# Optimization experiments

Measured on AMD Instinct MI355X. Metric: run time of the kernel, lower is better.

Reference implementation:

```python
import jax, jax.numpy as jnp
import numpy as np

S, I, IN_DIM, PROJ_DIM, OUT_DIM = 128, 384, 256, 32, 128
LN_EPS = 1e-5


def _layer_norm(x):
    # utils.normalize in OmegaFold: F.layer_norm over last dim, no affine params
    mu = jnp.mean(x, axis=-1, keepdims=True)
    var = jnp.var(x, axis=-1, keepdims=True)
    return (x - mu) * jax.lax.rsqrt(var + LN_EPS)


def setup_inputs() -> dict:
    key = jax.random.key(0)
    k0, k1, k2, k3 = jax.random.split(key, 4)
    node_repr = jax.random.normal(k0, (S, I, IN_DIM), dtype=jnp.float32)
    mask = (jax.random.uniform(k1, (S, I)) < 0.9).astype(jnp.float32)
    W_proj = jax.random.normal(k2, (IN_DIM, 2 * PROJ_DIM), dtype=jnp.float32) / np.sqrt(IN_DIM)
    b_proj = jnp.zeros((2 * PROJ_DIM,), dtype=jnp.float32)
    out_weights = jax.random.normal(k3, (PROJ_DIM, PROJ_DIM, OUT_DIM), dtype=jnp.float32) * 0.02
    out_bias = jnp.zeros((OUT_DIM,), dtype=jnp.float32)
    return {
        "node_repr": node_repr,
        "mask": mask,
        "W_proj": W_proj,
        "b_proj": b_proj,
        "out_weights": out_weights,
        "out_bias": out_bias,
    }


def reference(node_repr, mask, W_proj, b_proj, out_weights, out_bias):
    # LayerNorm (no affine) -> linear projection to 2*proj_dim
    x = _layer_norm(node_repr)                       # [s, i, in_dim]
    act = x @ W_proj + b_proj                        # [s, i, 2d]
    m = mask[..., None]                              # [s, i, 1]
    act = act * m
    # mask-pair counts: einsum('si,sj->ij')
    norm = jnp.einsum("si,sj->ij", mask, mask)[..., None]  # [i, j, 1]
    l = act[..., :PROJ_DIM]                          # [s, i, d]
    r = act[..., PROJ_DIM:]                          # [s, j, e]
    # outer-product mean over s, then contract (d,e)->f with the 3-tensor
    outer = jnp.einsum("sid,sje->ijde", l, r)        # [i, j, d, e]
    out = jnp.einsum("ijde,def->ijf", outer, out_weights) + out_bias  # [i, j, f]
    return out / (norm + 0.001)
```

## Files before the change

kernel.cpp:

```cpp
#include <hip/hip_runtime.h>

#define S_DIM 128
#define I_DIM 384
#define IN_DIM 256
#define PD 32
#define ODIM 128

typedef __attribute__((ext_vector_type(8))) __bf16 bf16x8;
typedef __attribute__((ext_vector_type(4))) float f32x4;

#define MFMA16(a, b, c) __builtin_amdgcn_mfma_f32_16x16x32_bf16((a), (b), (c), 0, 0, 0)

__device__ inline unsigned short f2bf(float f) {
    unsigned int u = __builtin_bit_cast(unsigned int, f);
    unsigned int r = (u + 0x7FFFu + ((u >> 16) & 1u)) >> 16;
    return (unsigned short)r;
}

__global__ void prep_cast(const float* __restrict__ Wp, const float* __restrict__ W2,
                          unsigned short* __restrict__ WpT, unsigned short* __restrict__ W2t) {
    int t = blockIdx.x * 256 + threadIdx.x;
    if (t < 64 * 256) {
        int f = t >> 8, k = t & 255;
        WpT[t] = f2bf(Wp[k * 64 + f]);
    }
    if (t < 128 * 1024) {
        int f = t >> 10, de = t & 1023;
        int e = de >> 5, d = de & 31;
        W2t[t] = f2bf(W2[(d * 32 + e) * 128 + f]);
    }
}

__global__ void norm_kernel(const float* __restrict__ mask, float* __restrict__ invn) {
    __shared__ float mi[S_DIM][16];
    __shared__ float mj[S_DIM][16];
    int t = threadIdx.x;
    int i0 = blockIdx.y * 16, j0 = blockIdx.x * 16;
    for (int p = 0; p < 8; ++p) {
        int s = p * 16 + (t >> 4);
        int c = t & 15;
        mi[s][c] = mask[s * I_DIM + i0 + c];
        mj[s][c] = mask[s * I_DIM + j0 + c];
    }
    __syncthreads();
    int ii = t >> 4, jj = t & 15;
    float acc = 0.f;
#pragma unroll 8
    for (int s = 0; s < S_DIM; ++s) acc += mi[s][ii] * mj[s][jj];
    invn[(i0 + ii) * I_DIM + (j0 + jj)] = 1.0f / (acc + 0.001f);
}

__global__ __launch_bounds__(256, 2) void ln_proj(const float* __restrict__ x,
                                                  const float* __restrict__ mask,
                                                  const float* __restrict__ bias,
                                                  const unsigned short* __restrict__ WpT_g,
                                                  unsigned short* __restrict__ lT,
                                                  unsigned short* __restrict__ rT) {
    __shared__ unsigned short xsh[64 * 264];
    __shared__ unsigned short wpT[64 * 264];
    int t = threadIdx.x;
    int w = t >> 6, lane = t & 63;
    int i = blockIdx.x >> 1;
    int s0 = (blockIdx.x & 1) * 64;

    {
        int f = t >> 2, kq = (t & 3) * 64;
#pragma unroll
        for (int p = 0; p < 8; ++p) {
            int k = kq + p * 8;
            *(uint4*)&wpT[f * 264 + k] = *(const uint4*)&WpT_g[f * 256 + k];
        }
    }

    float4 vbuf[4];
#pragma unroll
    for (int p = 0; p < 4; ++p)
        vbuf[p] = *(const float4*)(x + ((size_t)(s0 + w * 16 + p) * I_DIM + i) * IN_DIM + lane * 4);

    for (int it = 0; it < 16; ++it) {
        float4 v = vbuf[it & 3];
        if (it + 4 < 16)
            vbuf[it & 3] = *(const float4*)(x + ((size_t)(s0 + w * 16 + it + 4) * I_DIM + i) * IN_DIM + lane * 4);
        float s1 = v.x + v.y + v.z + v.w;
        float s2 = v.x * v.x + v.y * v.y + v.z * v.z + v.w * v.w;
#pragma unroll
        for (int off = 32; off >= 1; off >>= 1) {
            s1 += __shfl_xor(s1, off);
            s2 += __shfl_xor(s2, off);
        }
        float mu = s1 * (1.f / 256.f);
        float var = s2 * (1.f / 256.f) - mu * mu;
        float rs = rsqrtf(var + 1e-5f);
        unsigned int h0 = f2bf((v.x - mu) * rs);
        unsigned int h1 = f2bf((v.y - mu) * rs);
        unsigned int h2 = f2bf((v.z - mu) * rs);
        unsigned int h3 = f2bf((v.w - mu) * rs);
        uint2 pk;
        pk.x = h0 | (h1 << 16);
        pk.y = h2 | (h3 << 16);
        *(uint2*)&xsh[(w * 16 + it) * 264 + lane * 4] = pk;
    }
    __syncthreads();

    int l15 = lane & 15, q = lane >> 4;
    f32x4 acc[4];
#pragma unroll
    for (int nt = 0; nt < 4; ++nt) acc[nt] = (f32x4){0.f, 0.f, 0.f, 0.f};

    for (int k0 = 0; k0 < 256; k0 += 32) {
        bf16x8 a = *(bf16x8*)&xsh[(w * 16 + l15) * 264 + k0 + q * 8];
#pragma unroll
        for (int nt = 0; nt < 4; ++nt) {
            bf16x8 b = *(bf16x8*)&wpT[(nt * 16 + l15) * 264 + k0 + q * 8];
            acc[nt] = MFMA16(a, b, acc[nt]);
        }
    }

    float mval[4];
#pragma unroll
    for (int reg = 0; reg < 4; ++reg)
        mval[reg] = mask[(size_t)(s0 + w * 16 + q * 4 + reg) * I_DIM + i];

    __syncthreads();
    unsigned short* trsh = xsh;

#pragma unroll
    for (int nt = 0; nt < 4; ++nt) {
        int f = nt * 16 + l15;
        float bv = bias[f];
        unsigned int lo = (unsigned int)f2bf((acc[nt][0] + bv) * mval[0]) |
                          ((unsigned int)f2bf((acc[nt][1] + bv) * mval[1]) << 16);
        unsigned int hi = (unsigned int)f2bf((acc[nt][2] + bv) * mval[2]) |
                          ((unsigned int)f2bf((acc[nt][3] + bv) * mval[3]) << 16);
        uint2 pk; pk.x = lo; pk.y = hi;
        *(uint2*)&trsh[f * 72 + w * 16 + q * 4] = pk;
    }
    __syncthreads();

    {
        int fr = t >> 2, so = (t & 3) * 16;
        unsigned short* dst = ((fr < 32) ? lT : rT) + ((size_t)(i * 32 + (fr & 31)) * 128 + s0 + so);
        *(uint4*)dst = *(uint4*)&trsh[fr * 72 + so];
        *(uint4*)(dst + 8) = *(uint4*)&trsh[fr * 72 + so + 8];
    }
}

__global__ __launch_bounds__(256, 4) void outer_kernel(const unsigned short* __restrict__ lT,
                                                       const unsigned short* __restrict__ rT,
                                                       unsigned short* __restrict__ Gp,
                                                       int ib0) {
    __shared__ unsigned short sh[128 * 136];
    int t = threadIdx.x;
    int bx = blockIdx.x, by = blockIdx.y;
    int colL0 = (ib0 + by) * 128, colR0 = bx * 128;
    int w = t >> 6, lane = t & 63, l15 = lane & 15, q = lane >> 4;

    const unsigned short* lbase = lT + (size_t)(colL0 + w * 32 + l15) * 128 + q * 8;
    bf16x8 a0 = *(const bf16x8*)(lbase);
    bf16x8 a1 = *(const bf16x8*)(lbase + 16 * 128);

    {
        int m0 = t >> 3, c0 = (t & 7) * 8;
        const unsigned short* rbase = rT + (size_t)(colR0 + m0) * 128 + c0;
#pragma unroll
        for (int p = 0; p < 4; ++p) {
            *(uint4*)&sh[(m0 + p * 32) * 136 + c0] = *(const uint4*)(rbase + (size_t)p * 32 * 128);
            *(uint4*)&sh[(m0 + p * 32) * 136 + c0 + 64] = *(const uint4*)(rbase + (size_t)p * 32 * 128 + 64);
        }
    }
    __syncthreads();

    f32x4 acc[2][8];
#pragma unroll
    for (int mt = 0; mt < 2; ++mt)
#pragma unroll
        for (int nt = 0; nt < 8; ++nt) acc[mt][nt] = (f32x4){0.f, 0.f, 0.f, 0.f};

#pragma unroll
    for (int k0 = 0; k0 < 4; ++k0) {
        bf16x8 na0 = a0, na1 = a1;
        if (k0 < 3) {
            na0 = *(const bf16x8*)(lbase + (k0 + 1) * 32);
            na1 = *(const bf16x8*)(lbase + 16 * 128 + (k0 + 1) * 32);
        }
#pragma unroll
        for (int nt = 0; nt < 8; ++nt) {
            bf16x8 b = *(bf16x8*)&sh[(nt * 16 + l15) * 136 + k0 * 32 + q * 8];
            acc[0][nt] = MFMA16(a0, b, acc[0][nt]);
            acc[1][nt] = MFMA16(a1, b, acc[1][nt]);
        }
        a0 = na0; a1 = na1;
    }
    __syncthreads();

#pragma unroll
    for (int mt = 0; mt < 2; ++mt) {
        int rowb = w * 32 + mt * 16 + q * 4;
        int chnk = rowb >> 3;
        int win = rowb & 7;
#pragma unroll
        for (int nt = 0; nt < 8; ++nt) {
            int col = nt * 16 + l15;
            int cs = chnk ^ (col >> 5);
            unsigned int lo = (unsigned int)f2bf(acc[mt][nt][0]) | ((unsigned int)f2bf(acc[mt][nt][1]) << 16);
            unsigned int hi = (unsigned int)f2bf(acc[mt][nt][2]) | ((unsigned int)f2bf(acc[mt][nt][3]) << 16);
            uint2 pk; pk.x = lo; pk.y = hi;
            *(uint2*)&sh[col * 136 + cs * 8 + win] = pk;
        }
    }
    __syncthreads();

#pragma unroll
    for (int p8 = 0; p8 < 8; ++p8) {
        int g = p8 * 256 + t;
        int pair_loc = g >> 7;
        int c16 = g & 127;
        int i_loc = pair_loc >> 2, j_loc = pair_loc & 3;
        int e = c16 >> 2;
        int n = j_loc * 32 + e;
        int cs = (i_loc * 4 + (c16 & 3)) ^ j_loc;
        uint4 v = *(uint4*)&sh[n * 136 + cs * 8];
        size_t row = (size_t)(by * 4 + i_loc) * I_DIM + bx * 4 + j_loc;
        *(uint4*)&Gp[row * 1024 + (size_t)c16 * 8] = v;
    }
}

__global__ __launch_bounds__(256, 4) void contract_kernel(const unsigned short* __restrict__ Gp,
                                                          const unsigned short* __restrict__ W2t,
                                                          const float* __restrict__ invn,
                                                          const float* __restrict__ out_bias,
                                                          float* __restrict__ out,
                                                          int pair0) {
    __shared__ unsigned short Ash[2][64 * 40];
    int t = threadIdx.x;
    int w = t >> 6, lane = t & 63, l15 = lane & 15, q = lane >> 4;
    int p0 = blockIdx.x * 64;

    int sr = t >> 2, sc = (t & 3) * 8;
    const unsigned short* agp = Gp + (size_t)(p0 + sr) * 1024 + sc;
    *(uint4*)&Ash[0][sr * 40 + sc] = *(const uint4*)(agp);

    f32x4 acc[4][2];
#pragma unroll
    for (int mt = 0; mt < 4; ++mt) {
        acc[mt][0] = (f32x4){0.f, 0.f, 0.f, 0.f};
        acc[mt][1] = (f32x4){0.f, 0.f, 0.f, 0.f};
    }
    const unsigned short* wb0 = W2t + (size_t)(w * 32 + l15) * 1024 + q * 8;
    const unsigned short* wb1 = wb0 + 16 * 1024;

    bf16x8 b0c = *(const bf16x8*)(wb0);
    bf16x8 b1c = *(const bf16x8*)(wb1);
    __syncthreads();

    for (int k0 = 0; k0 < 32; ++k0) {
        int cur = k0 & 1;
        uint4 nxtA;
        bf16x8 b0n = b0c, b1n = b1c;
        if (k0 < 31) {
            nxtA = *(const uint4*)(agp + (k0 + 1) * 32);
            b0n = *(const bf16x8*)(wb0 + (k0 + 1) * 32);
            b1n = *(const bf16x8*)(wb1 + (k0 + 1) * 32);
        }
        bf16x8 a[4];
#pragma unroll
        for (int mt = 0; mt < 4; ++mt)
            a[mt] = *(bf16x8*)&Ash[cur][(mt * 16 + l15) * 40 + q * 8];
#pragma unroll
        for (int mt = 0; mt < 4; ++mt) {
            acc[mt][0] = MFMA16(a[mt], b0c, acc[mt][0]);
            acc[mt][1] = MFMA16(a[mt], b1c, acc[mt][1]);
        }
        if (k0 < 31) *(uint4*)&Ash[1 - cur][sr * 40 + sc] = nxtA;
        b0c = b0n; b1c = b1n;
        __syncthreads();
    }

#pragma unroll
    for (int u = 0; u < 2; ++u) {
        int f = w * 32 + u * 16 + l15;
        float bv = out_bias[f];
#pragma unroll
        for (int mt = 0; mt < 4; ++mt) {
#pragma unroll
            for (int reg = 0; reg < 4; ++reg) {
                int pl = pair0 + p0 + mt * 16 + q * 4 + reg;
                out[(size_t)pl * 128 + f] = (acc[mt][u][reg] + bv) * invn[pl];
            }
        }
    }
}

extern "C" void kernel_launch(void* const* d_in, const int* in_sizes, int n_in,
                              void* d_out, int out_size, void* d_ws, size_t ws_size,
                              hipStream_t stream) {
    const float* node = (const float*)d_in[0];
    const float* mask = (const float*)d_in[1];
    const float* Wp   = (const float*)d_in[2];
    const float* bp   = (const float*)d_in[3];
    const float* W2   = (const float*)d_in[4];
    const float* bo   = (const float*)d_in[5];
    float* out = (float*)d_out;

    char* ws = (char*)d_ws;
    unsigned short* lT  = (unsigned short*)(ws);
    unsigned short* rT  = (unsigned short*)(ws + 3145728);
    unsigned short* W2t = (unsigned short*)(ws + 6291456);
    unsigned short* WpT = (unsigned short*)(ws + 6553600);
    float*          inv = (float*)(ws + 6586368);
    unsigned short* Gp  = (unsigned short*)(ws + 8388608);

    int slab_i = 96;
    while (slab_i > 12 && 8388608ull + (size_t)slab_i * 384 * 1024 * 2 > ws_size) slab_i >>= 1;
    int nslab = 384 / slab_i;

    hipLaunchKernelGGL(prep_cast, dim3(512), dim3(256), 0, stream, Wp, W2, WpT, W2t);
    hipLaunchKernelGGL(norm_kernel, dim3(24, 24), dim3(256), 0, stream, mask, inv);
    hipLaunchKernelGGL(ln_proj, dim3(768), dim3(256), 0, stream, node, mask, bp, WpT, lT, rT);

    for (int s = 0; s < nslab; ++s) {
        hipLaunchKernelGGL(outer_kernel, dim3(96, slab_i / 4), dim3(256), 0, stream,
                           lT, rT, Gp, s * (slab_i / 4));
        hipLaunchKernelGGL(contract_kernel, dim3(slab_i * 384 / 64), dim3(256), 0, stream,
                           Gp, W2t, inv, bo, out, s * slab_i * I_DIM);
    }
}
```

Measured before the change: 332.3 us.

## Fuse outer-product and weight contraction into one kernel keeping pairs in LDS

Merges the outer-product kernel and the contraction kernel into a single kernel. Each block computes a 8x4 tile of (i,j) pairs, stores the 1024-wide outer products as bf16 in swizzled shared memory, then contracts against W2 with the K dimension split across the four waves. Partial sums are reduced through LDS before the bias and normalisation are applied. This removes the large Gp intermediate written to and read back from global memory, plus the slab launch loop. In exchange it uses 64KB of LDS and more registers, lowering occupancy to two blocks, and each block reloads W2 from global or cache.

```diff
diff --git a/kernel.cpp b/kernel.cpp
--- a/kernel.cpp
+++ b/kernel.cpp
@@ -145,23 +145,23 @@
     }
 }
 
-__global__ __launch_bounds__(256, 4) void outer_kernel(const unsigned short* __restrict__ lT,
+__global__ __launch_bounds__(256, 2) void fused_kernel(const unsigned short* __restrict__ lT,
                                                        const unsigned short* __restrict__ rT,
-                                                       unsigned short* __restrict__ Gp,
-                                                       int ib0) {
-    __shared__ unsigned short sh[128 * 136];
+                                                       const unsigned short* __restrict__ W2t,
+                                                       const float* __restrict__ invn,
+                                                       const float* __restrict__ out_bias,
+                                                       float* __restrict__ out) {
+    __shared__ unsigned short sh[32768];
     int t = threadIdx.x;
-    int bx = blockIdx.x, by = blockIdx.y;
-    int colL0 = (ib0 + by) * 128, colR0 = bx * 128;
     int w = t >> 6, lane = t & 63, l15 = lane & 15, q = lane >> 4;
-
-    const unsigned short* lbase = lT + (size_t)(colL0 + w * 32 + l15) * 128 + q * 8;
-    bf16x8 a0 = *(const bf16x8*)(lbase);
-    bf16x8 a1 = *(const bf16x8*)(lbase + 16 * 128);
+    int bx = blockIdx.x;
+    int by = blockIdx.y;
+    int wm = w >> 1, wn = w & 1;
+    char* shb = (char*)sh;
 
     {
         int m0 = t >> 3, c0 = (t & 7) * 8;
-        const unsigned short* rbase = rT + (size_t)(colR0 + m0) * 128 + c0;
+        const unsigned short* rbase = rT + (size_t)(bx * 128 + m0) * 128 + c0;
 #pragma unroll
         for (int p = 0; p < 4; ++p) {
             *(uint4*)&sh[(m0 + p * 32) * 136 + c0] = *(const uint4*)(rbase + (size_t)p * 32 * 128);
@@ -170,124 +170,107 @@
     }
     __syncthreads();
 
-    f32x4 acc[2][8];
-#pragma unroll
-    for (int mt = 0; mt < 2; ++mt)
-#pragma unroll
-        for (int nt = 0; nt < 8; ++nt) acc[mt][nt] = (f32x4){0.f, 0.f, 0.f, 0.f};
+    f32x4 acc[8][4];
+#pragma unroll
+    for (int mt = 0; mt < 8; ++mt)
+#pragma unroll
+        for (int nt = 0; nt < 4; ++nt) acc[mt][nt] = (f32x4){0.f, 0.f, 0.f, 0.f};
+
+    const unsigned short* lbase = lT + (size_t)(by * 256 + wm * 128 + l15) * 128 + q * 8;
+
+    bf16x8 a[8];
+#pragma unroll
+    for (int mt = 0; mt < 8; ++mt) a[mt] = *(const bf16x8*)(lbase + mt * 2048);
 
 #pragma unroll
     for (int k0 = 0; k0 < 4; ++k0) {
-        bf16x8 na0 = a0, na1 = a1;
+        bf16x8 na[8];
         if (k0 < 3) {
-            na0 = *(const bf16x8*)(lbase + (k0 + 1) * 32);
-            na1 = *(const bf16x8*)(lbase + 16 * 128 + (k0 + 1) * 32);
-        }
-#pragma unroll
-        for (int nt = 0; nt < 8; ++nt) {
-            bf16x8 b = *(bf16x8*)&sh[(nt * 16 + l15) * 136 + k0 * 32 + q * 8];
-            acc[0][nt] = MFMA16(a0, b, acc[0][nt]);
-            acc[1][nt] = MFMA16(a1, b, acc[1][nt]);
-        }
-        a0 = na0; a1 = na1;
-    }
-    __syncthreads();
-
-#pragma unroll
-    for (int mt = 0; mt < 2; ++mt) {
-        int rowb = w * 32 + mt * 16 + q * 4;
-        int chnk = rowb >> 3;
-        int win = rowb & 7;
-#pragma unroll
-        for (int nt = 0; nt < 8; ++nt) {
-            int col = nt * 16 + l15;
-            int cs = chnk ^ (col >> 5);
+#pragma unroll
+            for (int mt = 0; mt < 8; ++mt)
+                na[mt] = *(const bf16x8*)(lbase + mt * 2048 + (k0 + 1) * 32);
+        }
+#pragma unroll
+        for (int nt = 0; nt < 4; ++nt) {
+            bf16x8 b = *(bf16x8*)&sh[(wn * 64 + nt * 16 + l15) * 136 + k0 * 32 + q * 8];
+#pragma unroll
+            for (int mt = 0; mt < 8; ++mt)
+                acc[mt][nt] = MFMA16(a[mt], b, acc[mt][nt]);
+        }
+        if (k0 < 3) {
+#pragma unroll
+            for (int mt = 0; mt < 8; ++mt) a[mt] = na[mt];
+        }
+    }
+    __syncthreads();
+
+#pragma unroll
+    for (int mt = 0; mt < 8; ++mt) {
+        int i_loc = wm * 4 + (mt >> 1);
+        int dbase = (mt & 1) * 16 + q * 4;
+#pragma unroll
+        for (int nt = 0; nt < 4; ++nt) {
+            int j_loc = wn * 2 + (nt >> 1);
+            int e = (nt & 1) * 16 + l15;
+            int pair = i_loc * 4 + j_loc;
+            int kk = e * 32 + dbase;
             unsigned int lo = (unsigned int)f2bf(acc[mt][nt][0]) | ((unsigned int)f2bf(acc[mt][nt][1]) << 16);
             unsigned int hi = (unsigned int)f2bf(acc[mt][nt][2]) | ((unsigned int)f2bf(acc[mt][nt][3]) << 16);
             uint2 pk; pk.x = lo; pk.y = hi;
-            *(uint2*)&sh[col * 136 + cs * 8 + win] = pk;
-        }
-    }
-    __syncthreads();
-
-#pragma unroll
-    for (int p8 = 0; p8 < 8; ++p8) {
-        int g = p8 * 256 + t;
-        int pair_loc = g >> 7;
-        int c16 = g & 127;
-        int i_loc = pair_loc >> 2, j_loc = pair_loc & 3;
-        int e = c16 >> 2;
-        int n = j_loc * 32 + e;
-        int cs = (i_loc * 4 + (c16 & 3)) ^ j_loc;
-        uint4 v = *(uint4*)&sh[n * 136 + cs * 8];
-        size_t row = (size_t)(by * 4 + i_loc) * I_DIM + bx * 4 + j_loc;
-        *(uint4*)&Gp[row * 1024 + (size_t)c16 * 8] = v;
-    }
-}
-
-__global__ __launch_bounds__(256, 4) void contract_kernel(const unsigned short* __restrict__ Gp,
-                                                          const unsigned short* __restrict__ W2t,
-                                                          const float* __restrict__ invn,
-                                                          const float* __restrict__ out_bias,
-                                                          float* __restrict__ out,
-                                                          int pair0) {
-    __shared__ unsigned short Ash[2][64 * 40];
-    int t = threadIdx.x;
-    int w = t >> 6, lane = t & 63, l15 = lane & 15, q = lane >> 4;
-    int p0 = blockIdx.x * 64;
-
-    int sr = t >> 2, sc = (t & 3) * 8;
-    const unsigned short* agp = Gp + (size_t)(p0 + sr) * 1024 + sc;
-    *(uint4*)&Ash[0][sr * 40 + sc] = *(const uint4*)(agp);
-
-    f32x4 acc[4][2];
-#pragma unroll
-    for (int mt = 0; mt < 4; ++mt) {
-        acc[mt][0] = (f32x4){0.f, 0.f, 0.f, 0.f};
-        acc[mt][1] = (f32x4){0.f, 0.f, 0.f, 0.f};
-    }
-    const unsigned short* wb0 = W2t + (size_t)(w * 32 + l15) * 1024 + q * 8;
-    const unsigned short* wb1 = wb0 + 16 * 1024;
-
-    bf16x8 b0c = *(const bf16x8*)(wb0);
-    bf16x8 b1c = *(const bf16x8*)(wb1);
-    __syncthreads();
-
-    for (int k0 = 0; k0 < 32; ++k0) {
-        int cur = k0 & 1;
-        uint4 nxtA;
-        bf16x8 b0n = b0c, b1n = b1c;
-        if (k0 < 31) {
-            nxtA = *(const uint4*)(agp + (k0 + 1) * 32);
-            b0n = *(const bf16x8*)(wb0 + (k0 + 1) * 32);
-            b1n = *(const bf16x8*)(wb1 + (k0 + 1) * 32);
-        }
-        bf16x8 a[4];
-#pragma unroll
-        for (int mt = 0; mt < 4; ++mt)
-            a[mt] = *(bf16x8*)&Ash[cur][(mt * 16 + l15) * 40 + q * 8];
-#pragma unroll
-        for (int mt = 0; mt < 4; ++mt) {
-            acc[mt][0] = MFMA16(a[mt], b0c, acc[mt][0]);
-            acc[mt][1] = MFMA16(a[mt], b1c, acc[mt][1]);
-        }
-        if (k0 < 31) *(uint4*)&Ash[1 - cur][sr * 40 + sc] = nxtA;
-        b0c = b0n; b1c = b1n;
-        __syncthreads();
-    }
-
-#pragma unroll
-    for (int u = 0; u < 2; ++u) {
-        int f = w * 32 + u * 16 + l15;
-        float bv = out_bias[f];
-#pragma unroll
-        for (int mt = 0; mt < 4; ++mt) {
+            *(uint2*)(shb + pair * 2048 + ((kk * 2) ^ ((pair & 7) << 4))) = pk;
+        }
+    }
+    __syncthreads();
+
+    f32x4 acc3[2][8];
+#pragma unroll
+    for (int mt = 0; mt < 2; ++mt)
+#pragma unroll
+        for (int nt = 0; nt < 8; ++nt) acc3[mt][nt] = (f32x4){0.f, 0.f, 0.f, 0.f};
+
+    const unsigned short* wbase = W2t + (size_t)l15 * 1024 + q * 8;
+
+    for (int kq = 0; kq < 8; ++kq) {
+        int k0 = w * 8 + kq;
+        bf16x8 bfr[8];
+#pragma unroll
+        for (int nt = 0; nt < 8; ++nt)
+            bfr[nt] = *(const bf16x8*)(wbase + (size_t)nt * 16384 + k0 * 32);
+        int swz = ((k0 * 64 + q * 16) ^ ((l15 & 7) << 4));
+        bf16x8 a0 = *(bf16x8*)(shb + l15 * 2048 + swz);
+        bf16x8 a1 = *(bf16x8*)(shb + (16 + l15) * 2048 + swz);
+#pragma unroll
+        for (int nt = 0; nt < 8; ++nt) {
+            acc3[0][nt] = MFMA16(a0, bfr[nt], acc3[0][nt]);
+            acc3[1][nt] = MFMA16(a1, bfr[nt], acc3[1][nt]);
+        }
+    }
+    __syncthreads();
+
+    float* shf = (float*)sh;
+#pragma unroll
+    for (int mt3 = 0; mt3 < 2; ++mt3) {
+#pragma unroll
+        for (int nt = 0; nt < 8; ++nt) {
 #pragma unroll
             for (int reg = 0; reg < 4; ++reg) {
-                int pl = pair0 + p0 + mt * 16 + q * 4 + reg;
-                out[(size_t)pl * 128 + f] = (acc[mt][u][reg] + bv) * invn[pl];
+                int pair = mt3 * 16 + q * 4 + reg;
+                int f = nt * 16 + l15;
+                shf[w * 4096 + pair * 128 + (f ^ (((pair >> 2) & 1) << 4))] = acc3[mt3][nt][reg];
             }
         }
+    }
+    __syncthreads();
+
+#pragma unroll 4
+    for (int it = 0; it < 16; ++it) {
+        int v = it * 256 + t;
+        int pair = v >> 7, f = v & 127;
+        int idx = pair * 128 + (f ^ (((pair >> 2) & 1) << 4));
+        float s = shf[idx] + shf[4096 + idx] + shf[8192 + idx] + shf[12288 + idx];
+        int gi = by * 8 + (pair >> 2);
+        int gj = bx * 4 + (pair & 3);
+        out[((size_t)gi * I_DIM + gj) * 128 + f] = (s + out_bias[f]) * invn[gi * I_DIM + gj];
     }
 }
 
@@ -308,20 +291,10 @@
     unsigned short* W2t = (unsigned short*)(ws + 6291456);
     unsigned short* WpT = (unsigned short*)(ws + 6553600);
     float*          inv = (float*)(ws + 6586368);
-    unsigned short* Gp  = (unsigned short*)(ws + 8388608);
-
-    int slab_i = 96;
-    while (slab_i > 12 && 8388608ull + (size_t)slab_i * 384 * 1024 * 2 > ws_size) slab_i >>= 1;
-    int nslab = 384 / slab_i;
 
     hipLaunchKernelGGL(prep_cast, dim3(512), dim3(256), 0, stream, Wp, W2, WpT, W2t);
     hipLaunchKernelGGL(norm_kernel, dim3(24, 24), dim3(256), 0, stream, mask, inv);
     hipLaunchKernelGGL(ln_proj, dim3(768), dim3(256), 0, stream, node, mask, bp, WpT, lT, rT);
-
-    for (int s = 0; s < nslab; ++s) {
-        hipLaunchKernelGGL(outer_kernel, dim3(96, slab_i / 4), dim3(256), 0, stream,
-                           lT, rT, Gp, s * (slab_i / 4));
-        hipLaunchKernelGGL(contract_kernel, dim3(slab_i * 384 / 64), dim3(256), 0, stream,
-                           Gp, W2t, inv, bo, out, s * slab_i * I_DIM);
-    }
-}
+    hipLaunchKernelGGL(fused_kernel, dim3(96, 48), dim3(256), 0, stream,
+                       lT, rT, W2t, inv, bo, out);
+}
```

Result: slower. 342.0 us (+2.9%).
